# Kernel optimization log

Hardware: AMD Instinct MI355X
Metric: run time of the kernel (lower is better)

The kernel has to match this reference:

```python
import jax, jax.numpy as jnp
import numpy as np

B, S, D, H = 2, 2048, 1024, 16
DH = D // H
NEG = -1000000.0


def setup_inputs() -> dict:
    key = jax.random.key(0)
    k1, k2, k3, k4, k5, k6 = jax.random.split(key, 6)
    query = jax.random.normal(k1, (B, S, D), dtype=jnp.float32)
    key_t = jax.random.normal(k2, (B, S, D), dtype=jnp.float32)
    value = jax.random.normal(k3, (B, S, D), dtype=jnp.float32)
    # causal boolean mask, broadcast to [B*H, S, S] as the torch module expects
    causal = jnp.tril(jnp.ones((S, S), dtype=bool))
    attn_mask = jnp.broadcast_to(causal, (B * H, S, S))
    WQ = jax.random.normal(k4, (D, D), dtype=jnp.float32) * 0.02
    WK = jax.random.normal(k5, (D, D), dtype=jnp.float32) * 0.02
    WV = jax.random.normal(k6, (D, D), dtype=jnp.float32) * 0.02
    return {"query": query, "key": key_t, "value": value,
            "attn_mask": attn_mask, "WQ": WQ, "WK": WK, "WV": WV}


def reference(query, key, value, attn_mask, WQ, WK, WV):
    b, s, d = query.shape
    h = attn_mask.shape[0] // b
    dh = d // h
    # Linear projections (bias=False) then torch's split(dim=2)+concat(dim=0)
    # == reshape to [b,s,h,dh] and move head axis to the front: [h,b,s,dh]
    q = (query @ WQ).reshape(b, s, h, dh).transpose(2, 0, 1, 3)
    k = (key @ WK).reshape(b, s, h, dh).transpose(2, 0, 1, 3)
    v = (value @ WV).reshape(b, s, h, dh).transpose(2, 0, 1, 3)
    mask = attn_mask.reshape(h, b, s, s)
    add_mask = jnp.where(mask, jnp.float32(0.0), jnp.float32(NEG))
    # NOTE: original adds the mask BEFORE dividing by sqrt(dh) (baddbmm then /=)
    scores = (jnp.einsum('hbqd,hbkd->hbqk', q, k) + add_mask) / jnp.float32(dh ** 0.5)
    p = jax.nn.softmax(scores, axis=-1)
    p = p * mask.astype(p.dtype)  # mask applied a second time post-softmax
    out = jnp.einsum('hbqk,hbkd->hbqd', p, v)  # [h,b,s,dh]
    # concat heads back on the feature dim: [b,s,d]
    return out.transpose(1, 2, 0, 3).reshape(b, s, d)
```

## Files before the change

### kernel.cpp

```cpp
#include <hip/hip_runtime.h>
#include <hip/hip_bf16.h>

#define B_  2
#define S_  2048
#define D_  1024
#define H_  16
#define DH_ 64
#define BH_ (B_ * H_)
#define M_  (B_ * S_)

typedef __bf16 bf16x8 __attribute__((ext_vector_type(8)));
typedef __bf16 bf16x4 __attribute__((ext_vector_type(4)));
typedef float  f32x4  __attribute__((ext_vector_type(4)));

__device__ __forceinline__ __bf16 to_bf16(float f) {
  union { float f; unsigned u; } un; un.f = f;
  unsigned r = un.u + 0x7FFFu + ((un.u >> 16) & 1u);
  union { unsigned short s; __bf16 b; } o;
  o.s = (unsigned short)(r >> 16);
  return o.b;
}

__device__ __forceinline__ uint2 pack4_rne(f32x4 v) {
  union { __bf16 b[4]; uint2 u; } o;
#pragma unroll
  for (int i = 0; i < 4; ++i) o.b[i] = to_bf16(v[i]);
  return o.u;
}

__device__ __forceinline__ unsigned pack2_fast(float lo, float hi) {
  return ((__float_as_uint(hi) + 0x8000u) & 0xFFFF0000u) |
         ((__float_as_uint(lo) + 0x8000u) >> 16);
}

__device__ __forceinline__ void async_load16(const __bf16* g, __bf16* l) {
  __builtin_amdgcn_global_load_lds(
      (const __attribute__((address_space(1))) void*)g,
      (__attribute__((address_space(3))) void*)l, 16, 0, 0);
}

__global__ __launch_bounds__(256) void convert_x_kernel(
    const float* __restrict__ q_in, const float* __restrict__ k_in,
    const float* __restrict__ v_in, __bf16* __restrict__ Xb) {
  const float* src = blockIdx.z == 0 ? q_in : (blockIdx.z == 1 ? k_in : v_in);
  __bf16* dst = Xb + (size_t)blockIdx.z * M_ * D_;
  const size_t i = ((size_t)blockIdx.x * 256 + threadIdx.x) * 4;
  const float4 f = *(const float4*)(src + i);
  bf16x4 o;
  o[0] = to_bf16(f.x); o[1] = to_bf16(f.y); o[2] = to_bf16(f.z); o[3] = to_bf16(f.w);
  *(bf16x4*)(dst + i) = o;
}

__global__ void transpose_w_kernel(const float* __restrict__ Wq,
                                   const float* __restrict__ Wk,
                                   const float* __restrict__ Wv,
                                   __bf16* __restrict__ WT) {
  __shared__ float tile[32][33];
  const float* src = blockIdx.z == 0 ? Wq : (blockIdx.z == 1 ? Wk : Wv);
  __bf16* dst = WT + (size_t)blockIdx.z * D_ * D_;
  const int tx = threadIdx.x, ty = threadIdx.y;
  const int j  = blockIdx.x * 32 + tx;
  const int k0 = blockIdx.y * 32;
#pragma unroll
  for (int i = 0; i < 32; i += 8)
    tile[ty + i][tx] = src[(size_t)(k0 + ty + i) * D_ + j];
  __syncthreads();
  const int jr = blockIdx.x * 32;
  const int kc = k0 + tx;
#pragma unroll
  for (int i = 0; i < 32; i += 8)
    dst[(size_t)(jr + ty + i) * D_ + kc] = to_bf16(tile[tx][ty + i]);
}

__global__ __launch_bounds__(256) void proj_kernel(
    const __bf16* __restrict__ Xb, const __bf16* __restrict__ WT,
    __bf16* __restrict__ Qo, __bf16* __restrict__ Ko, __bf16* __restrict__ VTo) {
  const int lane = threadIdx.x & 63;
  const int wave = threadIdx.x >> 6;
  const int lr   = lane & 15;
  const int quad = lane >> 4;
  const int wr   = wave >> 1;
  const int wc   = wave & 1;
  const int which = blockIdx.z;
  const __bf16* X  = Xb + (size_t)which * M_ * D_;
  const __bf16* Wt = WT + (size_t)which * D_ * D_;
  const int m0 = blockIdx.y * 128;
  const int n0 = blockIdx.x * 128;

  __shared__ __align__(16) __bf16 As[128 * 32];
  __shared__ __align__(16) __bf16 Bs[128 * 32];

  f32x4 acc[4][4];
#pragma unroll
  for (int a = 0; a < 4; ++a)
#pragma unroll
    for (int b = 0; b < 4; ++b)
      acc[a][b] = f32x4{0.f, 0.f, 0.f, 0.f};

  const int srow  = (lane >> 2);
  const int schnk = (lane & 3) * 8;

  for (int kt = 0; kt < D_ / 32; ++kt) {
    const int k0 = kt * 32;
#pragma unroll
    for (int r16 = 0; r16 < 2; ++r16) {
      const int row = wave * 32 + r16 * 16 + srow;
      async_load16(X  + (size_t)(m0 + row) * D_ + k0 + schnk,
                   As + (size_t)(wave * 32 + r16 * 16) * 32);
      async_load16(Wt + (size_t)(n0 + row) * D_ + k0 + schnk,
                   Bs + (size_t)(wave * 32 + r16 * 16) * 32);
    }
    __syncthreads();

    bf16x8 af[4], bfr[4];
#pragma unroll
    for (int mi = 0; mi < 4; ++mi)
      af[mi] = *(const bf16x8*)(As + (size_t)(wr * 64 + mi * 16 + lr) * 32 + quad * 8);
#pragma unroll
    for (int ni = 0; ni < 4; ++ni)
      bfr[ni] = *(const bf16x8*)(Bs + (size_t)(wc * 64 + ni * 16 + lr) * 32 + quad * 8);
    if (which != 2) {
#pragma unroll
      for (int mi = 0; mi < 4; ++mi)
#pragma unroll
        for (int ni = 0; ni < 4; ++ni)
          acc[mi][ni] = __builtin_amdgcn_mfma_f32_16x16x32_bf16(bfr[ni], af[mi], acc[mi][ni], 0, 0, 0);
    } else {
#pragma unroll
      for (int mi = 0; mi < 4; ++mi)
#pragma unroll
        for (int ni = 0; ni < 4; ++ni)
          acc[mi][ni] = __builtin_amdgcn_mfma_f32_16x16x32_bf16(af[mi], bfr[ni], acc[mi][ni], 0, 0, 0);
    }
    __syncthreads();
  }

  if (which != 2) {
    __bf16* dst = which == 0 ? Qo : Ko;
#pragma unroll
    for (int mi = 0; mi < 4; ++mi)
#pragma unroll
      for (int ni = 0; ni < 4; ++ni) {
        const int gm  = m0 + wr * 64 + mi * 16 + lr;
        const int gn0 = n0 + wc * 64 + ni * 16 + quad * 4;
        const int b   = gm >> 11;
        const int s   = gm & (S_ - 1);
        const int h   = gn0 >> 6;
        const int dh0 = gn0 & (DH_ - 1);
        const int bh  = b * H_ + h;
        *(uint2*)(dst + ((size_t)bh * S_ + s) * DH_ + dh0) = pack4_rne(acc[mi][ni]);
      }
  } else {
#pragma unroll
    for (int mi = 0; mi < 4; ++mi)
#pragma unroll
      for (int ni = 0; ni < 4; ++ni) {
        const int gm0 = m0 + wr * 64 + mi * 16 + quad * 4;
        const int gn  = n0 + wc * 64 + ni * 16 + lr;
        const int b   = gm0 >> 11;
        const int s0  = gm0 & (S_ - 1);
        const int h   = gn >> 6;
        const int dh  = gn & (DH_ - 1);
        const int bh  = b * H_ + h;
        *(uint2*)(VTo + ((size_t)bh * DH_ + dh) * S_ + s0) = pack4_rne(acc[mi][ni]);
      }
  }
}

__global__ __launch_bounds__(64) void attn_kernel(
    const __bf16* __restrict__ Q, const __bf16* __restrict__ K,
    const __bf16* __restrict__ VT, float* __restrict__ out) {
  const int lane = threadIdx.x;
  const int lr   = lane & 15;
  const int quad = lane >> 4;
  const int qt = (gridDim.x - 1) - blockIdx.x;
  const int bh = blockIdx.y;
  const int q0 = qt * 32;
  const __bf16* Qb = Q  + (size_t)bh * S_ * DH_;
  const __bf16* Kb = K  + (size_t)bh * S_ * DH_;
  const __bf16* Vb = VT + (size_t)bh * DH_ * S_;
  const float CEXP = 0.18033688011112042f;

  bf16x8 qa[2][2];
#pragma unroll
  for (int rt = 0; rt < 2; ++rt)
#pragma unroll
    for (int hh = 0; hh < 2; ++hh)
      qa[rt][hh] = *(const bf16x8*)(Qb + (size_t)(q0 + rt * 16 + lr) * DH_ + hh * 32 + quad * 8);

  f32x4 o[2][4];
#pragma unroll
  for (int rt = 0; rt < 2; ++rt)
#pragma unroll
    for (int dt = 0; dt < 4; ++dt) o[rt][dt] = f32x4{0.f, 0.f, 0.f, 0.f};
  float lsum[2] = {0.f, 0.f};

  __shared__ __align__(16) __bf16 Pb[32][68];

  const int ntiles = qt / 2 + 1;
  for (int kt = 0; kt < ntiles; ++kt) {
    const int k0 = kt * 64;
    const bool full = (k0 + 63) <= q0;
    const f32x4 zero = f32x4{0.f, 0.f, 0.f, 0.f};

    bf16x8 kb[4][2], vb[4][2];
#pragma unroll
    for (int c = 0; c < 4; ++c) {
      kb[c][0] = *(const bf16x8*)(Kb + (size_t)(k0 + c * 16 + lr) * DH_ + quad * 8);
      kb[c][1] = *(const bf16x8*)(Kb + (size_t)(k0 + c * 16 + lr) * DH_ + 32 + quad * 8);
    }
#pragma unroll
    for (int dt = 0; dt < 4; ++dt) {
      vb[dt][0] = *(const bf16x8*)(Vb + (size_t)(dt * 16 + lr) * S_ + k0 + quad * 8);
      vb[dt][1] = *(const bf16x8*)(Vb + (size_t)(dt * 16 + lr) * S_ + k0 + 32 + quad * 8);
    }

    f32x4 st[2][4];
#pragma unroll
    for (int c = 0; c < 4; ++c)
#pragma unroll
      for (int rt = 0; rt < 2; ++rt) {
        st[rt][c] = __builtin_amdgcn_mfma_f32_16x16x32_bf16(kb[c][0], qa[rt][0], zero,      0, 0, 0);
        st[rt][c] = __builtin_amdgcn_mfma_f32_16x16x32_bf16(kb[c][1], qa[rt][1], st[rt][c], 0, 0, 0);
      }

#pragma unroll
    for (int rt = 0; rt < 2; ++rt) {
      const int qrow = q0 + rt * 16 + lr;
#pragma unroll
      for (int c = 0; c < 4; ++c) {
        float p[4];
#pragma unroll
        for (int r = 0; r < 4; ++r) {
          const int key = k0 + c * 16 + quad * 4 + r;
          float pv = exp2f(st[rt][c][r] * CEXP);
          if (!full && key > qrow) pv = 0.f;
          p[r] = pv;
          lsum[rt] += pv;
        }
        uint2 w; w.x = pack2_fast(p[0], p[1]); w.y = pack2_fast(p[2], p[3]);
        *(uint2*)(&Pb[rt * 16 + lr][c * 16 + quad * 4]) = w;
      }
    }
    __syncthreads();

#pragma unroll
    for (int rt = 0; rt < 2; ++rt) {
      const bf16x8 pa0 = *(const bf16x8*)(&Pb[rt * 16 + lr][quad * 8]);
      const bf16x8 pa1 = *(const bf16x8*)(&Pb[rt * 16 + lr][32 + quad * 8]);
#pragma unroll
      for (int dt = 0; dt < 4; ++dt) {
        o[rt][dt] = __builtin_amdgcn_mfma_f32_16x16x32_bf16(pa0, vb[dt][0], o[rt][dt], 0, 0, 0);
        o[rt][dt] = __builtin_amdgcn_mfma_f32_16x16x32_bf16(pa1, vb[dt][1], o[rt][dt], 0, 0, 0);
      }
    }
    __syncthreads();
  }

  const int b = bh / H_;
  const int h = bh % H_;
#pragma unroll
  for (int rt = 0; rt < 2; ++rt) {
    float l = lsum[rt];
    l += __shfl_xor(l, 16);
    l += __shfl_xor(l, 32);
    const float inv = 1.0f / l;
#pragma unroll
    for (int r = 0; r < 4; ++r) {
      const float invr = __shfl(inv, quad * 4 + r);
      const int row = q0 + rt * 16 + quad * 4 + r;
      float* orow = out + ((size_t)(b * S_ + row)) * D_ + h * DH_;
#pragma unroll
      for (int dt = 0; dt < 4; ++dt)
        orow[dt * 16 + lr] = o[rt][dt][r] * invr;
    }
  }
}

extern "C" void kernel_launch(void* const* d_in, const int* in_sizes, int n_in,
                              void* d_out, int out_size, void* d_ws, size_t ws_size,
                              hipStream_t stream) {
  const float* q_in = (const float*)d_in[0];
  const float* k_in = (const float*)d_in[1];
  const float* v_in = (const float*)d_in[2];
  const float* wq   = (const float*)d_in[4];
  const float* wk   = (const float*)d_in[5];
  const float* wv   = (const float*)d_in[6];

  __bf16* ws  = (__bf16*)d_ws;
  __bf16* Xb  = ws;
  __bf16* WT  = Xb + (size_t)3 * M_ * D_;
  __bf16* Qo  = WT + (size_t)3 * D_ * D_;
  __bf16* Ko  = Qo + (size_t)BH_ * S_ * DH_;
  __bf16* VTo = Ko + (size_t)BH_ * S_ * DH_;
  float* outp = (float*)d_out;

  convert_x_kernel<<<dim3(M_ * D_ / 1024, 1, 3), 256, 0, stream>>>(q_in, k_in, v_in, Xb);
  transpose_w_kernel<<<dim3(D_ / 32, D_ / 32, 3), dim3(32, 8), 0, stream>>>(wq, wk, wv, WT);
  proj_kernel<<<dim3(D_ / 128, M_ / 128, 3), 256, 0, stream>>>(Xb, WT, Qo, Ko, VTo);
  attn_kernel<<<dim3(S_ / 32, BH_), 64, 0, stream>>>(Qo, Ko, VTo, outp);
}
```

Before: 774.9 us.

## Widen projection K-tile to 64 and prefetch next K tile in attention loop

The projection GEMM now stages 64-wide K slices in shared memory and runs two MFMA sub-steps per tile, which halves the number of barrier pairs and load phases over the K dimension. The attention kernel loads the first K tile before the loop and, during each iteration, issues global loads for the next K tile while softmax and the PV MFMAs run. This hides K load latency behind compute. In exchange it uses more shared memory in the projection and more registers in attention, which could lower occupancy.

Result: no change. 776.0 us (+0.1%).

```diff
diff --git a/kernel.cpp b/kernel.cpp
--- a/kernel.cpp
+++ b/kernel.cpp
@@ -87,8 +87,8 @@
   const int m0 = blockIdx.y * 128;
   const int n0 = blockIdx.x * 128;
 
-  __shared__ __align__(16) __bf16 As[128 * 32];
-  __shared__ __align__(16) __bf16 Bs[128 * 32];
+  __shared__ __align__(16) __bf16 As[128 * 64];
+  __shared__ __align__(16) __bf16 Bs[128 * 64];
 
   f32x4 acc[4][4];
 #pragma unroll
@@ -97,40 +97,43 @@
     for (int b = 0; b < 4; ++b)
       acc[a][b] = f32x4{0.f, 0.f, 0.f, 0.f};
 
-  const int srow  = (lane >> 2);
-  const int schnk = (lane & 3) * 8;
-
-  for (int kt = 0; kt < D_ / 32; ++kt) {
-    const int k0 = kt * 32;
-#pragma unroll
-    for (int r16 = 0; r16 < 2; ++r16) {
-      const int row = wave * 32 + r16 * 16 + srow;
+  const int srow8 = lane >> 3;
+  const int schnk = (lane & 7) * 8;
+
+  for (int kt = 0; kt < D_ / 64; ++kt) {
+    const int k0 = kt * 64;
+#pragma unroll
+    for (int r = 0; r < 4; ++r) {
+      const int row = wave * 32 + r * 8 + srow8;
       async_load16(X  + (size_t)(m0 + row) * D_ + k0 + schnk,
-                   As + (size_t)(wave * 32 + r16 * 16) * 32);
+                   As + (size_t)(wave * 32 + r * 8) * 64);
       async_load16(Wt + (size_t)(n0 + row) * D_ + k0 + schnk,
-                   Bs + (size_t)(wave * 32 + r16 * 16) * 32);
+                   Bs + (size_t)(wave * 32 + r * 8) * 64);
     }
     __syncthreads();
 
-    bf16x8 af[4], bfr[4];
-#pragma unroll
-    for (int mi = 0; mi < 4; ++mi)
-      af[mi] = *(const bf16x8*)(As + (size_t)(wr * 64 + mi * 16 + lr) * 32 + quad * 8);
-#pragma unroll
-    for (int ni = 0; ni < 4; ++ni)
-      bfr[ni] = *(const bf16x8*)(Bs + (size_t)(wc * 64 + ni * 16 + lr) * 32 + quad * 8);
-    if (which != 2) {
+#pragma unroll
+    for (int kh = 0; kh < 2; ++kh) {
+      bf16x8 af[4], bfr[4];
 #pragma unroll
       for (int mi = 0; mi < 4; ++mi)
-#pragma unroll
-        for (int ni = 0; ni < 4; ++ni)
-          acc[mi][ni] = __builtin_amdgcn_mfma_f32_16x16x32_bf16(bfr[ni], af[mi], acc[mi][ni], 0, 0, 0);
-    } else {
-#pragma unroll
-      for (int mi = 0; mi < 4; ++mi)
-#pragma unroll
-        for (int ni = 0; ni < 4; ++ni)
-          acc[mi][ni] = __builtin_amdgcn_mfma_f32_16x16x32_bf16(af[mi], bfr[ni], acc[mi][ni], 0, 0, 0);
+        af[mi] = *(const bf16x8*)(As + (size_t)(wr * 64 + mi * 16 + lr) * 64 + kh * 32 + quad * 8);
+#pragma unroll
+      for (int ni = 0; ni < 4; ++ni)
+        bfr[ni] = *(const bf16x8*)(Bs + (size_t)(wc * 64 + ni * 16 + lr) * 64 + kh * 32 + quad * 8);
+      if (which != 2) {
+#pragma unroll
+        for (int mi = 0; mi < 4; ++mi)
+#pragma unroll
+          for (int ni = 0; ni < 4; ++ni)
+            acc[mi][ni] = __builtin_amdgcn_mfma_f32_16x16x32_bf16(bfr[ni], af[mi], acc[mi][ni], 0, 0, 0);
+      } else {
+#pragma unroll
+        for (int mi = 0; mi < 4; ++mi)
+#pragma unroll
+          for (int ni = 0; ni < 4; ++ni)
+            acc[mi][ni] = __builtin_amdgcn_mfma_f32_16x16x32_bf16(af[mi], bfr[ni], acc[mi][ni], 0, 0, 0);
+      }
     }
     __syncthreads();
   }
@@ -198,31 +201,43 @@
   __shared__ __align__(16) __bf16 Pb[32][68];
 
   const int ntiles = qt / 2 + 1;
+
+  bf16x8 kb[4][2];
+#pragma unroll
+  for (int c = 0; c < 4; ++c) {
+    kb[c][0] = *(const bf16x8*)(Kb + (size_t)(c * 16 + lr) * DH_ + quad * 8);
+    kb[c][1] = *(const bf16x8*)(Kb + (size_t)(c * 16 + lr) * DH_ + 32 + quad * 8);
+  }
+
   for (int kt = 0; kt < ntiles; ++kt) {
     const int k0 = kt * 64;
     const bool full = (k0 + 63) <= q0;
     const f32x4 zero = f32x4{0.f, 0.f, 0.f, 0.f};
 
-    bf16x8 kb[4][2], vb[4][2];
-#pragma unroll
-    for (int c = 0; c < 4; ++c) {
-      kb[c][0] = *(const bf16x8*)(Kb + (size_t)(k0 + c * 16 + lr) * DH_ + quad * 8);
-      kb[c][1] = *(const bf16x8*)(Kb + (size_t)(k0 + c * 16 + lr) * DH_ + 32 + quad * 8);
-    }
+    f32x4 st[2][4];
+#pragma unroll
+    for (int c = 0; c < 4; ++c)
+#pragma unroll
+      for (int rt = 0; rt < 2; ++rt) {
+        st[rt][c] = __builtin_amdgcn_mfma_f32_16x16x32_bf16(kb[c][0], qa[rt][0], zero,      0, 0, 0);
+        st[rt][c] = __builtin_amdgcn_mfma_f32_16x16x32_bf16(kb[c][1], qa[rt][1], st[rt][c], 0, 0, 0);
+      }
+
+    bf16x8 vb[4][2];
 #pragma unroll
     for (int dt = 0; dt < 4; ++dt) {
       vb[dt][0] = *(const bf16x8*)(Vb + (size_t)(dt * 16 + lr) * S_ + k0 + quad * 8);
       vb[dt][1] = *(const bf16x8*)(Vb + (size_t)(dt * 16 + lr) * S_ + k0 + 32 + quad * 8);
     }
-
-    f32x4 st[2][4];
-#pragma unroll
-    for (int c = 0; c < 4; ++c)
-#pragma unroll
-      for (int rt = 0; rt < 2; ++rt) {
-        st[rt][c] = __builtin_amdgcn_mfma_f32_16x16x32_bf16(kb[c][0], qa[rt][0], zero,      0, 0, 0);
-        st[rt][c] = __builtin_amdgcn_mfma_f32_16x16x32_bf16(kb[c][1], qa[rt][1], st[rt][c], 0, 0, 0);
-      }
+    bf16x8 kbn[4][2];
+    if (kt + 1 < ntiles) {
+      const int kn = k0 + 64;
+#pragma unroll
+      for (int c = 0; c < 4; ++c) {
+        kbn[c][0] = *(const bf16x8*)(Kb + (size_t)(kn + c * 16 + lr) * DH_ + quad * 8);
+        kbn[c][1] = *(const bf16x8*)(Kb + (size_t)(kn + c * 16 + lr) * DH_ + 32 + quad * 8);
+      }
+    }
 
 #pragma unroll
     for (int rt = 0; rt < 2; ++rt) {
@@ -255,6 +270,11 @@
       }
     }
     __syncthreads();
+
+    if (kt + 1 < ntiles) {
+#pragma unroll
+      for (int c = 0; c < 4; ++c) { kb[c][0] = kbn[c][0]; kb[c][1] = kbn[c][1]; }
+    }
   }
 
   const int b = bh / H_;
```
